# Kernel tuning notes

Hardware: AMD Instinct MI355X
Metric: run time of the kernel (lower is better)

Reference implementation:

```python
import jax, jax.numpy as jnp
import numpy as np
from jax import lax

K = 3  # kernel size
PAD = K // 2


def _patches(x):
    # x: [B,C,H,W] -> [B,C,K*K,H,W] (zero-padded 'same' neighborhoods)
    B, C, H, W = x.shape
    xp = jnp.pad(x, ((0, 0), (0, 0), (PAD, PAD), (PAD, PAD)))
    ps = [xp[:, :, i:i + H, j:j + W] for i in range(K) for j in range(K)]
    return jnp.stack(ps, axis=2)


def pac_conv2d(x, guide, w, b):
    # Pixel-adaptive conv (pacnet, kernel_type='gaussian', not channel-wise).
    # adaptive kernel from guidance: exp(-0.5 * ||g_patch - g_center||^2)
    gp = _patches(guide)                      # [B,C,P,H,W]
    d2 = jnp.sum((gp - guide[:, :, None]) ** 2, axis=1)  # [B,P,H,W]
    kern = jnp.exp(-0.5 * d2)                 # [B,P,H,W]
    xp = _patches(x)                          # [B,Cin,P,H,W]
    wf = w.reshape(w.shape[0], w.shape[1], K * K)  # [Cout,Cin,P]
    out = jnp.einsum('bcphw,bphw,ocp->bohw', xp, kern, wf)
    return out + b[None, :, None, None]


def conv2d(x, w, b):
    out = lax.conv_general_dilated(x, w, (1, 1), 'SAME',
                                   dimension_numbers=('NCHW', 'OIHW', 'NCHW'))
    return out + b[None, :, None, None]


def setup_inputs() -> dict:
    key = jax.random.key(0)
    ks = jax.random.split(key, 10)
    B, C, H, W = 8, 64, 128, 128
    fan = C * K * K
    s = 1.0 / np.sqrt(fan)
    inp = {
        'x': jax.random.normal(ks[0], (B, C, H, W), jnp.float32),
        'edge': jax.random.normal(ks[1], (B, C, H, W), jnp.float32),
        'w_pac1': jax.random.normal(ks[2], (C, C, K, K), jnp.float32) * s,
        'b_pac1': jax.random.normal(ks[3], (C,), jnp.float32) * s,
        'w_pac2': jax.random.normal(ks[4], (C, C, K, K), jnp.float32) * s,
        'b_pac2': jax.random.normal(ks[5], (C,), jnp.float32) * s,
        'w_e1': jax.random.normal(ks[6], (C, C, K, K), jnp.float32) * s,
        'b_e1': jax.random.normal(ks[7], (C,), jnp.float32) * s,
        'w_e2': jax.random.normal(ks[8], (C, C, K, K), jnp.float32) * s,
        'b_e2': jax.random.normal(ks[9], (C,), jnp.float32) * s,
    }
    return inp


def reference(x, edge, w_pac1, b_pac1, w_pac2, b_pac2, w_e1, b_e1, w_e2, b_e2):
    res_scale = 1.0
    # i=0: pac conv on sr (guided by current edge), plain conv on edge
    res_sr = pac_conv2d(x, edge, w_pac1, b_pac1)
    res_edge = conv2d(edge, w_e1, b_e1)
    # i=1: activation on both
    res_sr = jax.nn.relu(res_sr)
    res_edge = jax.nn.relu(res_edge)
    # i=2: pac conv guided by updated edge, plain conv on edge
    res_sr = pac_conv2d(res_sr, res_edge, w_pac2, b_pac2)
    res_edge = conv2d(res_edge, w_e2, b_e2)
    # dual residual
    res_sr = x + res_sr * res_scale
    res_edge = edge + res_edge * res_scale
    return (res_sr, res_edge)
```

## Files before the change

### kernel.cpp

```cpp
#include <hip/hip_runtime.h>

typedef unsigned short u16;
typedef __attribute__((ext_vector_type(8))) short s8;
typedef __attribute__((ext_vector_type(4))) float f4;

#define B_  8
#define C_  64
#define H_  128
#define W_  128
#define HW_ (H_*W_)
#define PITCH 72
#define WSZ 36864


static __device__ __forceinline__ u16 f2bu(float f) {
    union { float f; unsigned u; } c; c.f = f;
    unsigned u = c.u;
    u += 0x7fffu + ((u >> 16) & 1u);
    return (u16)(u >> 16);
}
static __device__ __forceinline__ float bu2f(u16 u) {
    union { unsigned u; float f; } c; c.u = ((unsigned)u) << 16; return c.f;
}

__global__ __launch_bounds__(256) void wt_all(
    const float* __restrict__ w0, const float* __restrict__ w1,
    const float* __restrict__ w2, const float* __restrict__ w3,
    u16* __restrict__ dst)
{
    int idx = blockIdx.x*256 + threadIdx.x;
    int cid = blockIdx.y;
    const float* w = (cid == 0) ? w0 : (cid == 1) ? w1 : (cid == 2) ? w2 : w3;
    int p = idx >> 12, o = (idx >> 6) & 63, c = idx & 63;
    dst[(size_t)cid*WSZ + idx] = f2bu(w[((size_t)o*64 + c)*9 + p]);
}

static __device__ __forceinline__ void stage_tile(
    u16* __restrict__ s_t, const u16* __restrict__ src, int b, int th0, int tw0, int t)
{
    for (int i = t; i < 10*18*8; i += 256) {
        int pix = i >> 3, ch = i & 7;
        int rr = pix / 18, ww = pix - rr*18;
        int gr = th0 + rr - 1, gw = tw0 + ww - 1;
        uint4 v = {0u,0u,0u,0u};
        if ((unsigned)gr < (unsigned)H_ && (unsigned)gw < (unsigned)W_)
            v = *(const uint4*)(src + ((size_t)b*HW_ + gr*W_ + gw)*64 + ch*8);
        *(uint4*)(&s_t[pix*PITCH + ch*8]) = v;
    }
}

static __device__ __forceinline__ void stage_tile_f32(
    u16* __restrict__ s_t, const float* __restrict__ src, int b, int th0, int tw0, int t)
{
    const bool lok = (tw0 != 0);
    const bool rok = (tw0 != W_ - 16);
    for (int i = t; i < 320; i += 256) {
        const int cp = i & 31, rr = i >> 5;
        const int gr = th0 + rr - 1;
        const int c0 = cp * 2;
        float v0[18], v1[18];
        if ((unsigned)gr < (unsigned)H_) {
            const float* a0 = src + ((size_t)b*C_ + c0)*HW_ + (size_t)gr*W_ + tw0;
            const float* a1 = a0 + HW_;
            v0[0]  = lok ? a0[-1] : 0.f;
            v1[0]  = lok ? a1[-1] : 0.f;
#pragma unroll
            for (int g = 0; g < 4; ++g) {
                *(f4*)(v0 + 1 + g*4) = *(const f4*)(a0 + g*4);
                *(f4*)(v1 + 1 + g*4) = *(const f4*)(a1 + g*4);
            }
            v0[17] = rok ? a0[16] : 0.f;
            v1[17] = rok ? a1[16] : 0.f;
        } else {
#pragma unroll
            for (int j = 0; j < 18; ++j) { v0[j] = 0.f; v1[j] = 0.f; }
        }
#pragma unroll
        for (int j = 0; j < 18; ++j) {
            unsigned pk = (unsigned)f2bu(v0[j]) | ((unsigned)f2bu(v1[j]) << 16);
            *(unsigned*)(&s_t[(rr*18 + j)*PITCH + c0]) = pk;
        }
    }
}

template<bool PAC>
static __device__ __forceinline__ void conv_core(
    const u16* __restrict__ s_t, const float* __restrict__ s_k,
    const u16* __restrict__ w, const float* __restrict__ bias,
    f4 acc[2][4], int wvM, int wvN, int ln, int quad)
{
#pragma unroll
    for (int mf = 0; mf < 2; ++mf) {
        f4 bv;
#pragma unroll
        for (int r = 0; r < 4; ++r) bv[r] = bias[wvM*32 + mf*16 + quad*4 + r];
#pragma unroll
        for (int nf = 0; nf < 4; ++nf) acc[mf][nf] = bv;
    }

#pragma unroll
    for (int p = 0; p < 9; ++p) {
        const int dr = p / 3, dc = p - dr*3;
        s8 a[2][2];
#pragma unroll
        for (int mf = 0; mf < 2; ++mf)
#pragma unroll
            for (int kc = 0; kc < 2; ++kc)
                a[mf][kc] = *(const s8*)(w + (((size_t)p*64 + wvM*32 + mf*16 + ln)*64 + kc*32 + quad*8));
        s8 bfr[4][2];
#pragma unroll
        for (int nf = 0; nf < 4; ++nf) {
            const u16* base = &s_t[((wvN*4 + nf + dr)*18 + ln + dc)*PITCH];
#pragma unroll
            for (int kc = 0; kc < 2; ++kc)
                bfr[nf][kc] = *(const s8*)(base + kc*32 + quad*8);
        }
        if (PAC) {
            float kv[4];
#pragma unroll
            for (int nf = 0; nf < 4; ++nf)
                kv[nf] = s_k[p*128 + (wvN*4 + nf)*16 + ln];
#pragma unroll
            for (int mf = 0; mf < 2; ++mf)
#pragma unroll
                for (int nf = 0; nf < 4; ++nf) {
                    f4 d = {0.f, 0.f, 0.f, 0.f};
                    d = __builtin_amdgcn_mfma_f32_16x16x32_bf16(a[mf][0], bfr[nf][0], d, 0, 0, 0);
                    d = __builtin_amdgcn_mfma_f32_16x16x32_bf16(a[mf][1], bfr[nf][1], d, 0, 0, 0);
                    acc[mf][nf] += kv[nf] * d;
                }
        } else {
#pragma unroll
            for (int mf = 0; mf < 2; ++mf)
#pragma unroll
                for (int nf = 0; nf < 4; ++nf) {
                    acc[mf][nf] = __builtin_amdgcn_mfma_f32_16x16x32_bf16(a[mf][0], bfr[nf][0], acc[mf][nf], 0, 0, 0);
                    acc[mf][nf] = __builtin_amdgcn_mfma_f32_16x16x32_bf16(a[mf][1], bfr[nf][1], acc[mf][nf], 0, 0, 0);
                }
        }
    }
}

static __device__ __forceinline__ void store_t(
    u16* __restrict__ out, f4 acc[2][4], int b, int th0, int tw0,
    int wvM, int wvN, int ln, int quad)
{
#pragma unroll
    for (int mf = 0; mf < 2; ++mf)
#pragma unroll
        for (int nf = 0; nf < 4; ++nf) {
            f4 v = acc[mf][nf];
            ushort4 o;
            o.x = f2bu(fmaxf(v[0], 0.f)); o.y = f2bu(fmaxf(v[1], 0.f));
            o.z = f2bu(fmaxf(v[2], 0.f)); o.w = f2bu(fmaxf(v[3], 0.f));
            size_t pix = (size_t)b*HW_ + (th0 + wvN*4 + nf)*W_ + tw0 + ln;
            *(ushort4*)(out + pix*64 + wvM*32 + mf*16 + quad*4) = o;
        }
}

static __device__ __forceinline__ void store_f(
    float* __restrict__ out, const float* __restrict__ resid,
    f4 acc[2][4], int b, int th0, int tw0, int wvM, int wvN, int ln, int quad)
{
#pragma unroll
    for (int mf = 0; mf < 2; ++mf)
#pragma unroll
        for (int nf = 0; nf < 4; ++nf) {
#pragma unroll
            for (int r = 0; r < 4; ++r) {
                int och = wvM*32 + mf*16 + quad*4 + r;
                size_t idx = ((size_t)b*C_ + och)*HW_ + (th0 + wvN*4 + nf)*W_ + tw0 + ln;
                out[idx] = acc[mf][nf][r] + resid[idx];
            }
        }
}

template<bool STAGE1>
__global__ __launch_bounds__(256, 2) void fused_stage(
    const float* __restrict__ inA_f, const float* __restrict__ inB_f,
    const u16* __restrict__ inA_t, const u16* __restrict__ inB_t,
    const u16* __restrict__ wA, const u16* __restrict__ wB,
    const float* __restrict__ biasA, const float* __restrict__ biasB,
    const float* __restrict__ residA_f, const float* __restrict__ residB_f,
    u16* __restrict__ outA_t, u16* __restrict__ outB_t,
    float* __restrict__ outA_f, float* __restrict__ outB_f)
{
    __shared__ u16   s_tA[10*18*PITCH];
    __shared__ u16   s_tB[10*18*PITCH];
    __shared__ float s_k[9*128];

    const int t    = threadIdx.x;
    const int L    = blockIdx.x;
    const int b    = L & 7;
    const int tw0  = ((L >> 3) & 7) * 16;
    const int th0  = (L >> 6) * 8;
    const int wv   = t >> 6;
    const int wvM  = wv >> 1;
    const int wvN  = wv & 1;
    const int lane = t & 63;
    const int ln   = lane & 15;
    const int quad = lane >> 4;

    if (STAGE1) {
        stage_tile_f32(s_tA, inA_f, b, th0, tw0, t);
        stage_tile_f32(s_tB, inB_f, b, th0, tw0, t);
    } else {
        stage_tile(s_tA, inA_t, b, th0, tw0, t);
        stage_tile(s_tB, inB_t, b, th0, tw0, t);
    }
    __syncthreads();

    {
        const int px   = t & 127;
        const int half = t >> 7;
        const int p0   = half ? 5 : 0;
        const int np   = half ? 4 : 5;
        const int py   = px >> 4, pxc = px & 15;
        float d2[5];
#pragma unroll
        for (int k = 0; k < 5; ++k) d2[k] = 0.f;
        const u16* cb = &s_tA[((py+1)*18 + (pxc+1))*PITCH];
#pragma unroll 1
        for (int co = 0; co < 8; ++co) {
            s8 c8 = *(const s8*)(cb + co*8);
            float cf[8];
#pragma unroll
            for (int j = 0; j < 8; ++j) cf[j] = bu2f((u16)c8[j]);
#pragma unroll
            for (int k = 0; k < 5; ++k) {
                if (k < np) {
                    int p = p0 + k;
                    int dr = p / 3, dc = p - dr*3;
                    s8 n8 = *(const s8*)(&s_tA[((py + dr)*18 + pxc + dc)*PITCH + co*8]);
#pragma unroll
                    for (int j = 0; j < 8; ++j) {
                        float d = bu2f((u16)n8[j]) - cf[j];
                        d2[k] += d * d;
                    }
                }
            }
        }
#pragma unroll
        for (int k = 0; k < 5; ++k)
            if (k < np) s_k[(p0+k)*128 + px] = __expf(-0.5f * d2[k]);
    }

    {
        f4 acc[2][4];
        conv_core<false>(s_tA, nullptr, wA, biasA, acc, wvM, wvN, ln, quad);
        if (STAGE1) store_t(outA_t, acc, b, th0, tw0, wvM, wvN, ln, quad);
        else        store_f(outA_f, residA_f, acc, b, th0, tw0, wvM, wvN, ln, quad);
    }

    __syncthreads();

    {
        f4 acc[2][4];
        conv_core<true>(s_tB, s_k, wB, biasB, acc, wvM, wvN, ln, quad);
        if (STAGE1) store_t(outB_t, acc, b, th0, tw0, wvM, wvN, ln, quad);
        else        store_f(outB_f, residB_f, acc, b, th0, tw0, wvM, wvN, ln, quad);
    }
}

extern "C" void kernel_launch(void* const* d_in, const int* in_sizes, int n_in,
                              void* d_out, int out_size, void* d_ws, size_t ws_size,
                              hipStream_t stream)
{
    const float* x      = (const float*)d_in[0];
    const float* edge   = (const float*)d_in[1];
    const float* w_pac1 = (const float*)d_in[2];
    const float* b_pac1 = (const float*)d_in[3];
    const float* w_pac2 = (const float*)d_in[4];
    const float* b_pac2 = (const float*)d_in[5];
    const float* w_e1   = (const float*)d_in[6];
    const float* b_e1   = (const float*)d_in[7];
    const float* w_e2   = (const float*)d_in[8];
    const float* b_e2   = (const float*)d_in[9];

    float* out_sr   = (float*)d_out;
    float* out_edge = out_sr + (size_t)B_*C_*HW_;

    const size_t NT = (size_t)B_*HW_*64;
    u16* res_edge1_t = (u16*)d_ws;
    u16* res_sr1_t   = res_edge1_t + NT;
    u16* w_t         = res_sr1_t + NT;

    dim3 blk(256);

    wt_all<<<dim3(144, 4), blk, 0, stream>>>(w_e1, w_pac1, w_e2, w_pac2, w_t);

    fused_stage<true ><<<dim3(1024), blk, 0, stream>>>(
        edge, x, nullptr, nullptr,
        w_t + 0*WSZ, w_t + 1*WSZ, b_e1, b_pac1,
        nullptr, nullptr, res_edge1_t, res_sr1_t, nullptr, nullptr);
    fused_stage<false><<<dim3(1024), blk, 0, stream>>>(
        nullptr, nullptr, res_edge1_t, res_sr1_t,
        w_t + 2*WSZ, w_t + 3*WSZ, b_e2, b_pac2,
        edge, x, nullptr, nullptr, out_edge, out_sr);
}
```

Measured before the change: 256.1 us.

## Double block to 512 threads so plain and PAC convs run concurrently

Each block now has two 256-thread groups. One group stages and computes the plain conv on the edge tile while the other stages and computes the pixel-adaptive conv, instead of one 256-thread group doing both in sequence. The Gaussian kernel weights are spread across all 512 threads, and a barrier makes them visible before the PAC conv reads them. This doubles the threads per block and the register pressure under launch_bounds(512,2), which may cut occupancy or force spills.

```diff
diff --git a/kernel.cpp b/kernel.cpp
--- a/kernel.cpp
+++ b/kernel.cpp
@@ -36,9 +36,9 @@
 }
 
 static __device__ __forceinline__ void stage_tile(
-    u16* __restrict__ s_t, const u16* __restrict__ src, int b, int th0, int tw0, int t)
-{
-    for (int i = t; i < 10*18*8; i += 256) {
+    u16* __restrict__ s_t, const u16* __restrict__ src, int b, int th0, int tw0, int tl)
+{
+    for (int i = tl; i < 10*18*8; i += 256) {
         int pix = i >> 3, ch = i & 7;
         int rr = pix / 18, ww = pix - rr*18;
         int gr = th0 + rr - 1, gw = tw0 + ww - 1;
@@ -50,11 +50,11 @@
 }
 
 static __device__ __forceinline__ void stage_tile_f32(
-    u16* __restrict__ s_t, const float* __restrict__ src, int b, int th0, int tw0, int t)
+    u16* __restrict__ s_t, const float* __restrict__ src, int b, int th0, int tw0, int tl)
 {
     const bool lok = (tw0 != 0);
     const bool rok = (tw0 != W_ - 16);
-    for (int i = t; i < 320; i += 256) {
+    for (int i = tl; i < 320; i += 256) {
         const int cp = i & 31, rr = i >> 5;
         const int gr = th0 + rr - 1;
         const int c0 = cp * 2;
@@ -176,7 +176,7 @@
 }
 
 template<bool STAGE1>
-__global__ __launch_bounds__(256, 2) void fused_stage(
+__global__ __launch_bounds__(512, 2) void fused_stage(
     const float* __restrict__ inA_f, const float* __restrict__ inB_f,
     const u16* __restrict__ inA_t, const u16* __restrict__ inB_t,
     const u16* __restrict__ wA, const u16* __restrict__ wB,
@@ -194,31 +194,33 @@
     const int b    = L & 7;
     const int tw0  = ((L >> 3) & 7) * 16;
     const int th0  = (L >> 6) * 8;
-    const int wv   = t >> 6;
+    const int grp  = t >> 8;
+    const int tl   = t & 255;
+    const int wv   = tl >> 6;
     const int wvM  = wv >> 1;
     const int wvN  = wv & 1;
-    const int lane = t & 63;
+    const int lane = tl & 63;
     const int ln   = lane & 15;
     const int quad = lane >> 4;
 
     if (STAGE1) {
-        stage_tile_f32(s_tA, inA_f, b, th0, tw0, t);
-        stage_tile_f32(s_tB, inB_f, b, th0, tw0, t);
+        if (grp == 0) stage_tile_f32(s_tA, inA_f, b, th0, tw0, tl);
+        else          stage_tile_f32(s_tB, inB_f, b, th0, tw0, tl);
     } else {
-        stage_tile(s_tA, inA_t, b, th0, tw0, t);
-        stage_tile(s_tB, inB_t, b, th0, tw0, t);
+        if (grp == 0) stage_tile(s_tA, inA_t, b, th0, tw0, tl);
+        else          stage_tile(s_tB, inB_t, b, th0, tw0, tl);
     }
     __syncthreads();
 
     {
-        const int px   = t & 127;
-        const int half = t >> 7;
-        const int p0   = half ? 5 : 0;
-        const int np   = half ? 4 : 5;
-        const int py   = px >> 4, pxc = px & 15;
-        float d2[5];
-#pragma unroll
-        for (int k = 0; k < 5; ++k) d2[k] = 0.f;
+        const int px = t & 127;
+        const int q  = t >> 7;
+        const int p0 = q * 2;
+        const int np = (q == 3) ? 3 : 2;
+        const int py = px >> 4, pxc = px & 15;
+        float d2[3];
+#pragma unroll
+        for (int k = 0; k < 3; ++k) d2[k] = 0.f;
         const u16* cb = &s_tA[((py+1)*18 + (pxc+1))*PITCH];
 #pragma unroll 1
         for (int co = 0; co < 8; ++co) {
@@ -227,7 +229,7 @@
 #pragma unroll
             for (int j = 0; j < 8; ++j) cf[j] = bu2f((u16)c8[j]);
 #pragma unroll
-            for (int k = 0; k < 5; ++k) {
+            for (int k = 0; k < 3; ++k) {
                 if (k < np) {
                     int p = p0 + k;
                     int dr = p / 3, dc = p - dr*3;
@@ -241,20 +243,17 @@
             }
         }
 #pragma unroll
-        for (int k = 0; k < 5; ++k)
+        for (int k = 0; k < 3; ++k)
             if (k < np) s_k[(p0+k)*128 + px] = __expf(-0.5f * d2[k]);
     }
-
-    {
+    __syncthreads();
+
+    if (grp == 0) {
         f4 acc[2][4];
         conv_core<false>(s_tA, nullptr, wA, biasA, acc, wvM, wvN, ln, quad);
         if (STAGE1) store_t(outA_t, acc, b, th0, tw0, wvM, wvN, ln, quad);
         else        store_f(outA_f, residA_f, acc, b, th0, tw0, wvM, wvN, ln, quad);
-    }
-
-    __syncthreads();
-
-    {
+    } else {
         f4 acc[2][4];
         conv_core<true>(s_tB, s_k, wB, biasB, acc, wvM, wvN, ln, quad);
         if (STAGE1) store_t(outB_t, acc, b, th0, tw0, wvM, wvN, ln, quad);
@@ -285,15 +284,13 @@
     u16* res_sr1_t   = res_edge1_t + NT;
     u16* w_t         = res_sr1_t + NT;
 
-    dim3 blk(256);
-
-    wt_all<<<dim3(144, 4), blk, 0, stream>>>(w_e1, w_pac1, w_e2, w_pac2, w_t);
-
-    fused_stage<true ><<<dim3(1024), blk, 0, stream>>>(
+    wt_all<<<dim3(144, 4), dim3(256), 0, stream>>>(w_e1, w_pac1, w_e2, w_pac2, w_t);
+
+    fused_stage<true ><<<dim3(1024), dim3(512), 0, stream>>>(
         edge, x, nullptr, nullptr,
         w_t + 0*WSZ, w_t + 1*WSZ, b_e1, b_pac1,
         nullptr, nullptr, res_edge1_t, res_sr1_t, nullptr, nullptr);
-    fused_stage<false><<<dim3(1024), blk, 0, stream>>>(
+    fused_stage<false><<<dim3(1024), dim3(512), 0, stream>>>(
         nullptr, nullptr, res_edge1_t, res_sr1_t,
         w_t + 2*WSZ, w_t + 3*WSZ, b_e2, b_pac2,
         edge, x, nullptr, nullptr, out_edge, out_sr);
```

Result: slower. 276.1 us (+7.8%).
